# Performance work log

Measured on AMD Instinct MI355X. Metric: run time of the kernel, lower is better.

## Reference

```python
import jax, jax.numpy as jnp
import numpy as np

DIMS = 1024
STATE = 2 * DIMS
EPS = 1e-8


def _rmsnorm(v, scale):
    # norm = ||v||_2 * d^{-1/2}
    d = v.shape[-1]
    n = jnp.sqrt(jnp.sum(v * v, axis=-1, keepdims=True)) * (d ** -0.5)
    return scale * v / (n + EPS)


def setup_inputs() -> dict:
    key = jax.random.key(0)
    ks = jax.random.split(key, 5)
    x = jax.random.normal(ks[0], (4, 2048, DIMS), dtype=jnp.float32)
    ls_scale = jnp.ones((DIMS // 2,), dtype=jnp.float32)
    rs_scale = jnp.ones((DIMS // 2,), dtype=jnp.float32)
    split_scale = jnp.full((DIMS,), 0.1, dtype=jnp.float32)
    sk = (1.0 / DIMS) ** 0.5
    Wk = jax.random.uniform(ks[1], (DIMS, STATE), jnp.float32, -sk, sk)
    Wugg = jax.random.uniform(ks[2], (DIMS, 3 * STATE), jnp.float32, -sk, sk)
    so = (1.0 / STATE) ** 0.5
    Wout = jax.random.uniform(ks[3], (STATE, DIMS), jnp.float32, -so, so)
    return {"x": x, "ls_scale": ls_scale, "rs_scale": rs_scale,
            "split_scale": split_scale, "Wk": Wk, "Wugg": Wugg, "Wout": Wout}


def reference(x, ls_scale, rs_scale, split_scale, Wk, Wugg, Wout):
    residual = x
    # RMS_split norm (output_dim=None)
    xl, xr = jnp.split(x, 2, axis=-1)
    xn = jnp.concatenate([_rmsnorm(xl, ls_scale), _rmsnorm(xr, rs_scale)], axis=-1)
    xn = xn * split_scale

    K = jax.nn.sigmoid(xn @ Wk)                      # [B,S,STATE]
    u, g_in, g_out = jnp.split(xn @ Wugg, 3, axis=-1)
    u = u * jax.nn.sigmoid(g_in) * (1.0 - K)

    # linear recurrence: h_0 = u_0; h_t = K_{t-1} * h_{t-1} + u_t
    a = jnp.concatenate([jnp.ones_like(K[..., :1, :]), K[..., :-1, :]], axis=-2)

    def combine(lhs, rhs):
        aL, bL = lhs
        aR, bR = rhs
        return (aL * aR, bL * aR + bR)

    _, h = jax.lax.associative_scan(combine, (a, u), axis=1)
    outputs = h * jax.nn.sigmoid(g_out)
    y = outputs @ Wout
    return y + residual
```

## Files before the change

### kernel.cpp

```cpp
#include <hip/hip_runtime.h>
#include <hip/hip_bf16.h>
#include <hip/hip_fp8.h>
#include <stdint.h>

#define DIMS 1024
#define STATE 2048
#define BATCH 4
#define SEQ 2048
#define TOKENS 8192
#define N1 8192
#define NCHUNK 16
#define CHUNKL (SEQ / NCHUNK)

typedef __hip_bfloat16 bf16;
typedef unsigned char u8;
typedef unsigned short u16;
typedef __attribute__((ext_vector_type(4))) float f32x4;
typedef __attribute__((ext_vector_type(16))) float f32x16;
typedef __attribute__((ext_vector_type(2))) long v2i64;
typedef __attribute__((ext_vector_type(4))) int v4i;
typedef __attribute__((ext_vector_type(8))) int v8i;

#define XN_SCALE 32.0f
#define W1_SCALE 256.0f
#define H_SCALE  32.0f
#define W2_SCALE 256.0f
#define INV_SCALE (1.0f / 8192.0f)

__device__ __forceinline__ float sigmoidf_(float x) {
  return 1.0f / (1.0f + __expf(-x));
}

__device__ __forceinline__ u8 to_fp8(float f) {
  __hip_fp8_e4m3 h(f);
  return h.__x;
}

__device__ __forceinline__ float b2f(u16 v) {
  union { uint32_t u; float f; } w;
  w.u = ((uint32_t)v) << 16;
  return w.f;
}

__device__ __forceinline__ u16 f2b(float f) {
  bf16 h = __float2bfloat16(f);
  return *(u16*)&h;
}

__device__ __forceinline__ void async_copy16(const void* g, void* l) {
  __builtin_amdgcn_global_load_lds(
      (const __attribute__((address_space(1))) void*)(uintptr_t)g,
      (__attribute__((address_space(3))) void*)(uint32_t)(uintptr_t)l,
      16, 0, 0);
}

__device__ __forceinline__ int swz32(int row, int kc) {
  int line = row >> 1;
  int sub = ((row & 1) << 2) | kc;
  return (line << 3) | (sub ^ (line & 7));
}
__device__ __forceinline__ void swz32_dec(int c, int& row, int& kc) {
  int line = c >> 3;
  int sub = (c & 7) ^ (line & 7);
  row = (line << 1) | (sub >> 2);
  kc = sub & 3;
}

__device__ __forceinline__ int xcd_swz(int wg, int nwg) {
  return (wg & 7) * (nwg >> 3) + (wg >> 3);
}

__global__ __launch_bounds__(256) void transpose_fp8_kernel(
    const float* __restrict__ W, u8* __restrict__ Wt, int K, int N,
    int stream_base, int interleave, float scale) {
  __shared__ float tile[32][33];
  int tx = threadIdx.x & 31;
  int ty = threadIdx.x >> 5;
  long col = (long)blockIdx.x * 32 + tx;
  long rowb = (long)blockIdx.y * 32;
#pragma unroll
  for (int i = 0; i < 32; i += 8)
    tile[ty + i][tx] = W[(rowb + ty + i) * N + col];
  __syncthreads();
  long ocol = rowb + tx;
  long orow = (long)blockIdx.x * 32 + ty;
#pragma unroll
  for (int i = 0; i < 32; i += 8) {
    long n = orow + i;
    long dstrow = interleave ? (((n & 2047) << 2) | (stream_base + (n >> 11))) : n;
    Wt[dstrow * K + ocol] = to_fp8(tile[tx][ty + i] * scale);
  }
}

__global__ __launch_bounds__(256) void rmsnorm_kernel(
    const float* __restrict__ x, const float* __restrict__ ls,
    const float* __restrict__ rs, const float* __restrict__ ss,
    u8* __restrict__ xn8) {
  int token = blockIdx.x;
  int tid = threadIdx.x;
  const float4* xt = (const float4*)(x + (long)token * DIMS);
  float4 v = xt[tid];
  float s = v.x * v.x + v.y * v.y + v.z * v.z + v.w * v.w;
#pragma unroll
  for (int d = 32; d > 0; d >>= 1) s += __shfl_down(s, d);
  __shared__ float parts[4];
  if ((tid & 63) == 0) parts[tid >> 6] = s;
  __syncthreads();
  int j = tid * 4;
  bool left = j < 512;
  float sum = left ? (parts[0] + parts[1]) : (parts[2] + parts[3]);
  float n = sqrtf(sum * (1.0f / 512.0f));
  float inv = 1.0f / (n + 1e-8f);
  const float4* sc = (const float4*)(left ? ls : rs);
  float4 g = sc[left ? tid : tid - 128];
  float4 p = ((const float4*)ss)[tid];
  u8 q[4];
  q[0] = to_fp8(v.x * g.x * inv * p.x * XN_SCALE);
  q[1] = to_fp8(v.y * g.y * inv * p.y * XN_SCALE);
  q[2] = to_fp8(v.z * g.z * inv * p.z * XN_SCALE);
  q[3] = to_fp8(v.w * g.w * inv * p.w * XN_SCALE);
  *(uint32_t*)(xn8 + (long)token * DIMS + j) = *(uint32_t*)q;
}

__device__ __forceinline__ void g1f8_stage(const u8* __restrict__ A,
                                           const u8* __restrict__ Bt,
                                           long arow0, long brow0, int k0,
                                           int wave, int lane, u8* As, u8* Bs) {
  const int K = DIMS;
#pragma unroll
  for (int i = 0; i < 4; i++) {
    int c = (wave * 4 + i) * 64 + lane;
    int row, kc; swz32_dec(c, row, kc);
    async_copy16(A + (arow0 + row) * K + k0 + kc * 16, (char*)As + (wave * 4 + i) * 1024);
  }
#pragma unroll
  for (int i = 0; i < 2; i++) {
    int c = (wave * 2 + i) * 64 + lane;
    int row, kc; swz32_dec(c, row, kc);
    async_copy16(Bt + (brow0 + row) * K + k0 + kc * 16, (char*)Bs + (wave * 2 + i) * 1024);
  }
}

__device__ __forceinline__ v8i ld_frag64(const u8* base, int row, int q4) {
  v4i lo = *(const v4i*)(base + swz32(row, q4 * 2) * 16);
  v4i hi = *(const v4i*)(base + swz32(row, q4 * 2 + 1) * 16);
  return __builtin_shufflevector(lo, hi, 0, 1, 2, 3, 4, 5, 6, 7);
}

__global__ __launch_bounds__(256, 2) void gemm1_fp8(
    const u8* __restrict__ A, const u8* __restrict__ Bt,
    uint32_t* __restrict__ AU, u16* __restrict__ GO) {
  __shared__ __align__(16) u8 As0[256 * 64], As1[256 * 64];
  __shared__ __align__(16) u8 Bs0[128 * 64], Bs1[128 * 64];
  __shared__ __align__(16) u8 occ_pad[8192];
  int tid = threadIdx.x;
  int lane = tid & 63, wave = tid >> 6;
  int wm = wave & 1, wn = wave >> 1;
  int wg = xcd_swz(blockIdx.y * gridDim.x + blockIdx.x, gridDim.x * gridDim.y);
  int bx = wg & 63;
  int by = wg >> 6;
  long arow0 = (long)by * 256;
  long brow0 = (long)bx * 128;
  int m_lane = lane & 31, q4 = lane >> 5;
  if (tid == 0) occ_pad[0] = 0;
  f32x16 acc[4][2] = {};

  g1f8_stage(A, Bt, arow0, brow0, 0, wave, lane, As0, Bs0);
  __syncthreads();

  for (int it = 0; it < 16; ++it) {
    const u8* Asc = (it & 1) ? As1 : As0;
    const u8* Bsc = (it & 1) ? Bs1 : Bs0;
    u8* Asn = (it & 1) ? As0 : As1;
    u8* Bsn = (it & 1) ? Bs0 : Bs1;
    if (it + 1 < 16)
      g1f8_stage(A, Bt, arow0, brow0, (it + 1) * 64, wave, lane, Asn, Bsn);
    v8i af[4], bf[2];
#pragma unroll
    for (int mt = 0; mt < 4; mt++)
      af[mt] = ld_frag64(Asc, wm * 128 + mt * 32 + m_lane, q4);
#pragma unroll
    for (int nt = 0; nt < 2; nt++)
      bf[nt] = ld_frag64(Bsc, wn * 64 + nt * 32 + m_lane, q4);
#pragma unroll
    for (int mt = 0; mt < 4; mt++)
#pragma unroll
      for (int nt = 0; nt < 2; nt++)
        acc[mt][nt] = __builtin_amdgcn_mfma_scale_f32_32x32x64_f8f6f4(
            bf[nt], af[mt], acc[mt][nt], 0, 0, 0, 127,
            0, 127);
    __syncthreads();
  }

#pragma unroll
  for (int mt = 0; mt < 4; mt++) {
    long row = arow0 + wm * 128 + mt * 32 + m_lane;
    long rb = row * STATE;
#pragma unroll
    for (int nt = 0; nt < 2; nt++) {
#pragma unroll
      for (int g = 0; g < 4; g++) {
        long col = brow0 + wn * 64 + nt * 32 + g * 8 + q4 * 4;
        long ch = col >> 2;
        float kraw = acc[mt][nt][g * 4 + 0] * INV_SCALE;
        float uraw = acc[mt][nt][g * 4 + 1] * INV_SCALE;
        float gin  = acc[mt][nt][g * 4 + 2] * INV_SCALE;
        float gout = acc[mt][nt][g * 4 + 3] * INV_SCALE;
        float ah = sigmoidf_(kraw);
        float uu = uraw * sigmoidf_(gin) * (1.0f - ah);
        u16 pr[2];
        pr[0] = f2b(ah);
        pr[1] = f2b(uu);
        AU[rb + ch] = *(uint32_t*)pr;
        GO[rb + ch] = f2b(sigmoidf_(gout));
      }
    }
  }
}

__device__ __forceinline__ void g2f8_stage(const u8* __restrict__ A,
                                           const u8* __restrict__ Bt,
                                           long arow0, long brow0, int k0,
                                           int wave, int lane, u8* As, u8* Bs) {
  const int K = STATE;
#pragma unroll
  for (int i = 0; i < 2; i++) {
    int c = (wave * 2 + i) * 64 + lane;
    int row, kc; swz32_dec(c, row, kc);
    async_copy16(A + (arow0 + row) * K + k0 + kc * 16, (char*)As + (wave * 2 + i) * 1024);
  }
#pragma unroll
  for (int i = 0; i < 2; i++) {
    int c = (wave * 2 + i) * 64 + lane;
    int row, kc; swz32_dec(c, row, kc);
    async_copy16(Bt + (brow0 + row) * K + k0 + kc * 16, (char*)Bs + (wave * 2 + i) * 1024);
  }
}

__global__ __launch_bounds__(256) void gemm2_fp8(
    const u8* __restrict__ A, const u8* __restrict__ Bt,
    float* __restrict__ C, const float* __restrict__ resid) {
  __shared__ __align__(16) u8 As[3][128 * 64];
  __shared__ __align__(16) u8 Bs[3][128 * 64];
  int tid = threadIdx.x;
  int lane = tid & 63, wave = tid >> 6;
  int wm = wave & 1, wn = wave >> 1;
  int wg = xcd_swz(blockIdx.y * gridDim.x + blockIdx.x, gridDim.x * gridDim.y);
  int bx = wg & (gridDim.x - 1);
  int by = wg >> 3;
  long arow0 = (long)by * 128;
  long brow0 = (long)bx * 128;
  int m_lane = lane & 31, q4 = lane >> 5;
  f32x16 acc[2][2] = {};

  g2f8_stage(A, Bt, arow0, brow0, 0, wave, lane, As[0], Bs[0]);
  g2f8_stage(A, Bt, arow0, brow0, 64, wave, lane, As[1], Bs[1]);

  int cur = 0, nxt = 2;
  for (int it = 0; it < 32; ++it) {
    if (it == 31) asm volatile("s_waitcnt vmcnt(0)" ::: "memory");
    else          asm volatile("s_waitcnt vmcnt(4)" ::: "memory");
    __builtin_amdgcn_s_barrier();
    __builtin_amdgcn_sched_barrier(0);
    if (it + 2 < 32)
      g2f8_stage(A, Bt, arow0, brow0, (it + 2) * 64, wave, lane, As[nxt], Bs[nxt]);
    const u8* Asc = As[cur];
    const u8* Bsc = Bs[cur];
    v8i af[2], bf[2];
#pragma unroll
    for (int mt = 0; mt < 2; mt++)
      af[mt] = ld_frag64(Asc, wm * 64 + mt * 32 + m_lane, q4);
#pragma unroll
    for (int nt = 0; nt < 2; nt++)
      bf[nt] = ld_frag64(Bsc, wn * 64 + nt * 32 + m_lane, q4);
    __builtin_amdgcn_s_setprio(1);
#pragma unroll
    for (int mt = 0; mt < 2; mt++)
#pragma unroll
      for (int nt = 0; nt < 2; nt++)
        acc[mt][nt] = __builtin_amdgcn_mfma_scale_f32_32x32x64_f8f6f4(
            bf[nt], af[mt], acc[mt][nt], 0, 0, 0, 127, 0, 127);
    __builtin_amdgcn_s_setprio(0);
    cur = cur == 2 ? 0 : cur + 1;
    nxt = nxt == 2 ? 0 : nxt + 1;
  }
#pragma unroll
  for (int mt = 0; mt < 2; mt++) {
    long row = arow0 + wm * 64 + mt * 32 + m_lane;
#pragma unroll
    for (int nt = 0; nt < 2; nt++) {
#pragma unroll
      for (int g = 0; g < 4; g++) {
        long col = brow0 + wn * 64 + nt * 32 + g * 8 + q4 * 4;
        float4 rv = *(const float4*)(resid + row * DIMS + col);
        float4 ov;
        ov.x = acc[mt][nt][g * 4 + 0] * INV_SCALE + rv.x;
        ov.y = acc[mt][nt][g * 4 + 1] * INV_SCALE + rv.y;
        ov.z = acc[mt][nt][g * 4 + 2] * INV_SCALE + rv.z;
        ov.w = acc[mt][nt][g * 4 + 3] * INV_SCALE + rv.w;
        *(float4*)(C + row * DIMS + col) = ov;
      }
    }
  }
}

__global__ __launch_bounds__(256) void chunk_summary_kernel(
    const uint32_t* __restrict__ AU, float* __restrict__ carryA,
    float* __restrict__ carryU) {
  int b = blockIdx.x;
  int ch = blockIdx.y * 256 + threadIdx.x;
  int chunk = blockIdx.z;
  int t0 = chunk * CHUNKL;
  const uint32_t* base = AU + (long)b * SEQ * STATE + ch;
  float ap = 1.0f;
  if (chunk != 0) ap = b2f((u16)(base[(long)(t0 - 1) * STATE] & 0xffff));
  float A = 1.0f, U = 0.0f;
#pragma unroll 8
  for (int t = t0; t < t0 + CHUNKL; t++) {
    uint32_t w = base[(long)t * STATE];
    float ah = b2f((u16)(w & 0xffff));
    float u  = b2f((u16)(w >> 16));
    A *= ap;
    U = ap * U + u;
    ap = ah;
  }
  int cidx = (b * NCHUNK + chunk) * STATE + ch;
  carryA[cidx] = A;
  carryU[cidx] = U;
}

__global__ __launch_bounds__(256) void carry_scan_kernel(
    const float* __restrict__ carryA, const float* __restrict__ carryU,
    float* __restrict__ carryIn) {
  int idx = blockIdx.x * 256 + threadIdx.x;
  int b = idx >> 11;
  int ch = idx & 2047;
  float h = 0.0f;
#pragma unroll
  for (int c = 0; c < NCHUNK; c++) {
    int cidx = (b * NCHUNK + c) * STATE + ch;
    carryIn[cidx] = h;
    h = carryA[cidx] * h + carryU[cidx];
  }
}

__global__ __launch_bounds__(256) void scan_chunk_kernel(
    const uint32_t* __restrict__ AU, const u16* __restrict__ GO,
    const float* __restrict__ carryIn, u8* __restrict__ sco8) {
  int b = blockIdx.x;
  int c0 = blockIdx.y * 32;
  int chunk = blockIdx.z;
  int tstart = chunk * CHUNKL;
  __shared__ float a_s[32][65], u_s[32][65], h_s[32][65];
  int tid = threadIdx.x;
  int lane = tid & 63, wave = tid >> 6;
  int cc = tid & 31;
  int tq = tid >> 5;

  float carryH[8], carryK[8];
#pragma unroll
  for (int i = 0; i < 8; i++) {
    int ch = c0 + wave * 8 + i;
    carryH[i] = carryIn[(b * NCHUNK + chunk) * STATE + ch];
    carryK[i] = (chunk == 0)
                    ? 1.0f
                    : b2f((u16)(AU[((long)(b * SEQ + tstart - 1)) * STATE + ch] & 0xffff));
  }

  float g_r[8];
  for (int t0 = tstart; t0 < tstart + CHUNKL; t0 += 64) {
#pragma unroll
    for (int i = 0; i < 8; i++) {
      int t = tq * 8 + i;
      long idx = ((long)(b * SEQ + t0 + t)) * STATE + c0 + cc;
      uint32_t w = AU[idx];
      a_s[cc][t] = b2f((u16)(w & 0xffff));
      u_s[cc][t] = b2f((u16)(w >> 16));
      g_r[i] = b2f(GO[idx]);
    }
    __syncthreads();
#pragma unroll
    for (int i = 0; i < 8; i++) {
      int ch = wave * 8 + i;
      float aK = a_s[ch][lane];
      float u = u_s[ch][lane];
      float a = __shfl_up(aK, 1);
      if (lane == 0) a = carryK[i];
      float A = a, U = u;
#pragma unroll
      for (int d = 1; d < 64; d <<= 1) {
        float Au = __shfl_up(A, d);
        float Uu = __shfl_up(U, d);
        if (lane >= d) { U += A * Uu; A *= Au; }
      }
      float h = U + A * carryH[i];
      carryH[i] = __shfl(h, 63);
      carryK[i] = __shfl(aK, 63);
      h_s[ch][lane] = h;
    }
    __syncthreads();
#pragma unroll
    for (int i = 0; i < 8; i++) {
      int t = tq * 8 + i;
      sco8[((long)(b * SEQ + t0 + t)) * STATE + c0 + cc] =
          to_fp8(h_s[cc][t] * g_r[i] * H_SCALE);
    }
    __syncthreads();
  }
}

extern "C" void kernel_launch(void* const* d_in, const int* in_sizes, int n_in,
                              void* d_out, int out_size, void* d_ws, size_t ws_size,
                              hipStream_t stream) {
  const float* x    = (const float*)d_in[0];
  const float* ls   = (const float*)d_in[1];
  const float* rs   = (const float*)d_in[2];
  const float* ss   = (const float*)d_in[3];
  const float* Wk   = (const float*)d_in[4];
  const float* Wugg = (const float*)d_in[5];
  const float* Wout = (const float*)d_in[6];
  float* out = (float*)d_out;

  char* ws = (char*)d_ws;
  u8*   W1f8 = (u8*)ws;
  u8*   W2f8 = (u8*)(ws + 8388608);
  u8*   xn8  = (u8*)(ws + 10485760);
  uint32_t* AU = (uint32_t*)(ws + 18874368);
  u16*  GOb  = (u16*)(ws + 18874368 + 67108864);
  u8*   sco8 = (u8*)(ws + 18874368 + 67108864 + 33554432);
  float* carryA  = (float*)xn8;
  float* carryU  = carryA + BATCH * NCHUNK * STATE;
  float* carryIn = carryU + BATCH * NCHUNK * STATE;

  transpose_fp8_kernel<<<dim3(STATE / 32, DIMS / 32), 256, 0, stream>>>(
      Wk, W1f8, DIMS, STATE, 0, 1, W1_SCALE);
  transpose_fp8_kernel<<<dim3(3 * STATE / 32, DIMS / 32), 256, 0, stream>>>(
      Wugg, W1f8, DIMS, 3 * STATE, 1, 1, W1_SCALE);
  transpose_fp8_kernel<<<dim3(DIMS / 32, STATE / 32), 256, 0, stream>>>(
      Wout, W2f8, STATE, DIMS, 0, 0, W2_SCALE);

  rmsnorm_kernel<<<TOKENS, 256, 0, stream>>>(x, ls, rs, ss, xn8);

  gemm1_fp8<<<dim3(N1 / 128, TOKENS / 256), 256, 0, stream>>>(xn8, W1f8, AU, GOb);

  chunk_summary_kernel<<<dim3(BATCH, STATE / 256, NCHUNK), 256, 0, stream>>>(
      AU, carryA, carryU);
  carry_scan_kernel<<<dim3(BATCH * STATE / 256), 256, 0, stream>>>(
      carryA, carryU, carryIn);
  scan_chunk_kernel<<<dim3(BATCH, STATE / 32, NCHUNK), 256, 0, stream>>>(
      AU, GOb, carryIn, sco8);

  gemm2_fp8<<<dim3(DIMS / 128, TOKENS / 128), 256, 0, stream>>>(
      sco8, W2f8, out, x);
}
```

Before: 384.6 us.

## Switch FP8 output GEMM to double-buffered BK=128 stages with syncthreads

The output-projection FP8 GEMM moves from a three-stage BK=64 async pipeline with explicit vmcnt waits to a two-buffer BK=128 pipeline. Each K row is stored as two virtual 64-byte rows so the existing swizzle and fragment loader still apply, and the loop runs 16 iterations of two MFMA sub-steps each. The intent is to halve the per-iteration barrier and loop overhead and add launch_bounds occupancy 2. LDS use rises to 64KB per block. The loop also drops the vmcnt-based waits and setprio in favour of __syncthreads, which may expose load latency.

```diff
diff --git a/kernel.cpp b/kernel.cpp
--- a/kernel.cpp
+++ b/kernel.cpp
@@ -224,24 +224,26 @@
                                            int wave, int lane, u8* As, u8* Bs) {
   const int K = STATE;
 #pragma unroll
-  for (int i = 0; i < 2; i++) {
-    int c = (wave * 2 + i) * 64 + lane;
-    int row, kc; swz32_dec(c, row, kc);
-    async_copy16(A + (arow0 + row) * K + k0 + kc * 16, (char*)As + (wave * 2 + i) * 1024);
-  }
-#pragma unroll
-  for (int i = 0; i < 2; i++) {
-    int c = (wave * 2 + i) * 64 + lane;
-    int row, kc; swz32_dec(c, row, kc);
-    async_copy16(Bt + (brow0 + row) * K + k0 + kc * 16, (char*)Bs + (wave * 2 + i) * 1024);
-  }
-}
-
-__global__ __launch_bounds__(256) void gemm2_fp8(
+  for (int i = 0; i < 4; i++) {
+    int c = (wave * 4 + i) * 64 + lane;
+    int vrow, kc; swz32_dec(c, vrow, kc);
+    async_copy16(A + (arow0 + (vrow >> 1)) * K + k0 + (vrow & 1) * 64 + kc * 16,
+                 (char*)As + (wave * 4 + i) * 1024);
+  }
+#pragma unroll
+  for (int i = 0; i < 4; i++) {
+    int c = (wave * 4 + i) * 64 + lane;
+    int vrow, kc; swz32_dec(c, vrow, kc);
+    async_copy16(Bt + (brow0 + (vrow >> 1)) * K + k0 + (vrow & 1) * 64 + kc * 16,
+                 (char*)Bs + (wave * 4 + i) * 1024);
+  }
+}
+
+__global__ __launch_bounds__(256, 2) void gemm2_fp8(
     const u8* __restrict__ A, const u8* __restrict__ Bt,
     float* __restrict__ C, const float* __restrict__ resid) {
-  __shared__ __align__(16) u8 As[3][128 * 64];
-  __shared__ __align__(16) u8 Bs[3][128 * 64];
+  __shared__ __align__(16) u8 As0[128 * 128], As1[128 * 128];
+  __shared__ __align__(16) u8 Bs0[128 * 128], Bs1[128 * 128];
   int tid = threadIdx.x;
   int lane = tid & 63, wave = tid >> 6;
   int wm = wave & 1, wn = wave >> 1;
@@ -253,36 +255,33 @@
   int m_lane = lane & 31, q4 = lane >> 5;
   f32x16 acc[2][2] = {};
 
-  g2f8_stage(A, Bt, arow0, brow0, 0, wave, lane, As[0], Bs[0]);
-  g2f8_stage(A, Bt, arow0, brow0, 64, wave, lane, As[1], Bs[1]);
-
-  int cur = 0, nxt = 2;
-  for (int it = 0; it < 32; ++it) {
-    if (it == 31) asm volatile("s_waitcnt vmcnt(0)" ::: "memory");
-    else          asm volatile("s_waitcnt vmcnt(4)" ::: "memory");
-    __builtin_amdgcn_s_barrier();
-    __builtin_amdgcn_sched_barrier(0);
-    if (it + 2 < 32)
-      g2f8_stage(A, Bt, arow0, brow0, (it + 2) * 64, wave, lane, As[nxt], Bs[nxt]);
-    const u8* Asc = As[cur];
-    const u8* Bsc = Bs[cur];
-    v8i af[2], bf[2];
-#pragma unroll
-    for (int mt = 0; mt < 2; mt++)
-      af[mt] = ld_frag64(Asc, wm * 64 + mt * 32 + m_lane, q4);
-#pragma unroll
-    for (int nt = 0; nt < 2; nt++)
-      bf[nt] = ld_frag64(Bsc, wn * 64 + nt * 32 + m_lane, q4);
-    __builtin_amdgcn_s_setprio(1);
-#pragma unroll
-    for (int mt = 0; mt < 2; mt++)
+  g2f8_stage(A, Bt, arow0, brow0, 0, wave, lane, As0, Bs0);
+  __syncthreads();
+
+  for (int it = 0; it < 16; ++it) {
+    const u8* Asc = (it & 1) ? As1 : As0;
+    const u8* Bsc = (it & 1) ? Bs1 : Bs0;
+    u8* Asn = (it & 1) ? As0 : As1;
+    u8* Bsn = (it & 1) ? Bs0 : Bs1;
+    if (it + 1 < 16)
+      g2f8_stage(A, Bt, arow0, brow0, (it + 1) * 128, wave, lane, Asn, Bsn);
+#pragma unroll
+    for (int ks = 0; ks < 2; ks++) {
+      v8i af[2], bf[2];
+#pragma unroll
+      for (int mt = 0; mt < 2; mt++)
+        af[mt] = ld_frag64(Asc, (wm * 64 + mt * 32 + m_lane) * 2 + ks, q4);
 #pragma unroll
       for (int nt = 0; nt < 2; nt++)
-        acc[mt][nt] = __builtin_amdgcn_mfma_scale_f32_32x32x64_f8f6f4(
-            bf[nt], af[mt], acc[mt][nt], 0, 0, 0, 127, 0, 127);
-    __builtin_amdgcn_s_setprio(0);
-    cur = cur == 2 ? 0 : cur + 1;
-    nxt = nxt == 2 ? 0 : nxt + 1;
+        bf[nt] = ld_frag64(Bsc, (wn * 64 + nt * 32 + m_lane) * 2 + ks, q4);
+#pragma unroll
+      for (int mt = 0; mt < 2; mt++)
+#pragma unroll
+        for (int nt = 0; nt < 2; nt++)
+          acc[mt][nt] = __builtin_amdgcn_mfma_scale_f32_32x32x64_f8f6f4(
+              bf[nt], af[mt], acc[mt][nt], 0, 0, 0, 127, 0, 127);
+    }
+    __syncthreads();
   }
 #pragma unroll
   for (int mt = 0; mt < 2; mt++) {
```

Result: no change. 379.1 us (-1.4%).
